# Performance work log

Hardware: AMD Instinct MI355X
Metric: run time of the kernel (lower is better)

Reference implementation:

```python
import jax, jax.numpy as jnp
import numpy as np

NUM_EXPERTS = 16
IN_FEATURES = 512
OUT_FEATURES = 512
N_TOKENS = 2048


def setup_inputs() -> dict:
    key = jax.random.key(0)
    k_x, k_idx, k_w, k_b = jax.random.split(key, 4)
    x = jax.random.normal(k_x, (N_TOKENS, IN_FEATURES), dtype=jnp.float32)
    indices = jax.random.randint(k_idx, (N_TOKENS,), 0, NUM_EXPERTS, dtype=jnp.int64)
    # nn.Linear default init: U(-1/sqrt(in), 1/sqrt(in)) for weight [out,in] and bias [out]
    bound = 1.0 / np.sqrt(IN_FEATURES)
    W = jax.random.uniform(k_w, (NUM_EXPERTS, OUT_FEATURES, IN_FEATURES),
                           minval=-bound, maxval=bound, dtype=jnp.float32)
    b = jax.random.uniform(k_b, (NUM_EXPERTS, OUT_FEATURES),
                           minval=-bound, maxval=bound, dtype=jnp.float32)
    return {"x": x, "indices": indices, "W": W, "b": b}


def reference(x, indices, W, b):
    # Faithful to SwitchLinear.forward: gather per-token expert weight/bias,
    # then per-token GEMV (batched matmul with a length-1 row dim).
    w_tok = W[indices]            # [N, out, in]  (naive per-token weight gather)
    b_tok = b[indices]            # [N, out]
    out = jnp.einsum('ni,noi->no', x, w_tok) + b_tok  # [N, out]
    return out
```

## Files before the change

### kernel.cpp

```cpp
#include <hip/hip_runtime.h>
#include <hip/hip_bf16.h>

#define NE    16
#define INF   512
#define OUTF  512
#define NT    2048
#define OTILE 32
#define TCH   64
#define WROWS OTILE
#define LSTRIDE 520

#define SZ_W   (WROWS * LSTRIDE * 2)
#define SZ_X   (TCH * LSTRIDE * 2)
#define SZ_LST ((NT + TCH) * 4)
#define SMEM_BYTES (SZ_W + SZ_X + SZ_LST + 32)

typedef __attribute__((ext_vector_type(4))) float f32x4;
typedef __attribute__((ext_vector_type(8))) short bf16x8;
typedef __attribute__((ext_vector_type(4))) short bf16x4;

__device__ inline short f2bf(float f) {
    union { __hip_bfloat16 h; short s; } u;
    u.h = __float2bfloat16(f);
    return u.s;
}

__device__ inline bf16x4 cvt4(f32x4 v) {
    bf16x4 r;
    r[0] = f2bf(v[0]); r[1] = f2bf(v[1]); r[2] = f2bf(v[2]); r[3] = f2bf(v[3]);
    return r;
}

__global__ __launch_bounds__(512, 2)
void switch_linear_kernel(const float* __restrict__ x,
                          const int* __restrict__ idx,
                          const float* __restrict__ W,
                          const float* __restrict__ bias,
                          float* __restrict__ out)
{
    extern __shared__ char smem[];
    short* s_W    = (short*)smem;
    short* s_X    = (short*)(smem + SZ_W);
    int*   s_list = (int*)(smem + SZ_W + SZ_X);
    int*   s_wcnt = (int*)(smem + SZ_W + SZ_X + SZ_LST);

    const int b   = blockIdx.x;
    const int e   = b & 15;
    const int oj  = (b >> 4) & 15;
    const int o0  = oj * OTILE;
    const int tid = threadIdx.x;
    const int lane = tid & 63;
    const int wid  = tid >> 6;

    int iv[4];
#pragma unroll
    for (int it = 0; it < 4; ++it)
        iv[it] = idx[wid * 256 + it * 64 + lane];

    const float* wbase = W + ((size_t)e * OUTF + o0) * INF;
#pragma unroll
    for (int i = 0; i < 8; ++i) {
        const int li = tid + i * 512;
        f32x4 v = ((const f32x4*)wbase)[li];
        const int fidx = li * 4;
        const int row = fidx >> 9;
        const int col = fidx & 511;
        *(bf16x4*)(&s_W[row * LSTRIDE + col]) = cvt4(v);
    }

    unsigned long long masks[4];
    int wtot = 0;
#pragma unroll
    for (int it = 0; it < 4; ++it) {
        const unsigned long long mk = __ballot(iv[it] == e);
        masks[it] = mk;
        wtot += __popcll(mk);
    }
    if (lane == 0) s_wcnt[wid] = wtot;
    __syncthreads();
    int base = 0;
#pragma unroll
    for (int w = 0; w < 8; ++w) { int c = s_wcnt[w]; if (w < wid) base += c; }
    const int cnt = s_wcnt[0] + s_wcnt[1] + s_wcnt[2] + s_wcnt[3]
                  + s_wcnt[4] + s_wcnt[5] + s_wcnt[6] + s_wcnt[7];
    const unsigned long long below = (1ull << lane) - 1ull;
    int run = base;
#pragma unroll
    for (int it = 0; it < 4; ++it) {
        const unsigned long long mk = masks[it];
        if (mk & (1ull << lane))
            s_list[run + __popcll(mk & below)] = wid * 256 + it * 64 + lane;
        run += __popcll(mk);
    }
    const int cnt_pad = (cnt + TCH - 1) & ~(TCH - 1);
    for (int i = cnt + tid; i < cnt_pad; i += 512) s_list[i] = -1;
    __syncthreads();
    if (cnt == 0) return;

    const int wt = wid >> 1;
    const int wo = wid & 1;
    const int lr = lane & 15;
    const int q  = lane >> 4;
    const int orow = o0 + wo * 16 + lr;

    bf16x8 bfr[16];
#pragma unroll
    for (int kk = 0; kk < 16; ++kk)
        bfr[kk] = *(const bf16x8*)(&s_W[(wo * 16 + lr) * LSTRIDE + kk * 32 + q * 8]);
    const float bv = bias[e * OUTF + orow];

    const int slot = tid >> 3;
    const int sub  = tid & 7;

    const int M = cnt_pad / TCH;
    int m0 = oj % M;
    for (int k = 0; k < M; ++k) {
        int m = m0 + k; if (m >= M) m -= M;
        const int cb = m * TCH;

        int tok_s = s_list[cb + slot];
        if (tok_s < 0) tok_s = 0;
        const f32x4* xr = (const f32x4*)(x + (size_t)tok_s * INF);
#pragma unroll
        for (int i = 0; i < 16; ++i) {
            f32x4 v = xr[sub + i * 8];
            *(bf16x4*)(&s_X[slot * LSTRIDE + sub * 4 + i * 32]) = cvt4(v);
        }
        __syncthreads();

        f32x4 acc = {0.f, 0.f, 0.f, 0.f};
#pragma unroll
        for (int kk = 0; kk < 16; ++kk) {
            bf16x8 afr = *(const bf16x8*)(&s_X[(wt * 16 + lr) * LSTRIDE + kk * 32 + q * 8]);
            acc = __builtin_amdgcn_mfma_f32_16x16x32_bf16(afr, bfr[kk], acc, 0, 0, 0);
        }
#pragma unroll
        for (int j = 0; j < 4; ++j) {
            const int tok = s_list[cb + wt * 16 + q * 4 + j];
            if (tok >= 0) out[(size_t)tok * OUTF + orow] = acc[j] + bv;
        }
        __syncthreads();
    }
}

extern "C" void kernel_launch(void* const* d_in, const int* in_sizes, int n_in,
                              void* d_out, int out_size, void* d_ws, size_t ws_size,
                              hipStream_t stream) {
    const float* x    = (const float*)d_in[0];
    const int*   idx  = (const int*)d_in[1];
    const float* W    = (const float*)d_in[2];
    const float* bias = (const float*)d_in[3];
    float* out = (float*)d_out;

    dim3 grid(NE * (OUTF / OTILE));
    dim3 block(512);
    switch_linear_kernel<<<grid, block, SMEM_BYTES, stream>>>(x, idx, W, bias, out);
}
```

Before: 14.24 us.

## Split token chunks across two blocks per expert tile with smaller blocks

Doubles the grid by adding a z dimension that splits each expert's token chunks between two blocks, halving block size to 256 threads and chunk size to 32 tokens. Each block still converts the full 32x512 weight tile and scans all indices, so that work is duplicated. The x loads are batched into registers before conversion to expose more memory parallelism, and the final barrier is skipped. The aim is more concurrent blocks and shorter per-block serial chains, at the cost of redundant weight staging and index scanning.

```diff
diff --git a/kernel.cpp b/kernel.cpp
--- a/kernel.cpp
+++ b/kernel.cpp
@@ -6,32 +6,33 @@
 #define OUTF  512
 #define NT    2048
 #define OTILE 32
-#define TCH   64
-#define WROWS OTILE
+#define TCH   32
+#define NZ    2
 #define LSTRIDE 520
 
-#define SZ_W   (WROWS * LSTRIDE * 2)
+#define SZ_W   (OTILE * LSTRIDE * 2)
 #define SZ_X   (TCH * LSTRIDE * 2)
 #define SZ_LST ((NT + TCH) * 4)
-#define SMEM_BYTES (SZ_W + SZ_X + SZ_LST + 32)
+#define SMEM_BYTES (SZ_W + SZ_X + SZ_LST + 64)
 
 typedef __attribute__((ext_vector_type(4))) float f32x4;
 typedef __attribute__((ext_vector_type(8))) short bf16x8;
 typedef __attribute__((ext_vector_type(4))) short bf16x4;
 
-__device__ inline short f2bf(float f) {
-    union { __hip_bfloat16 h; short s; } u;
+__device__ inline unsigned short f2bf(float f) {
+    union { __hip_bfloat16 h; unsigned short s; } u;
     u.h = __float2bfloat16(f);
     return u.s;
 }
 
 __device__ inline bf16x4 cvt4(f32x4 v) {
     bf16x4 r;
-    r[0] = f2bf(v[0]); r[1] = f2bf(v[1]); r[2] = f2bf(v[2]); r[3] = f2bf(v[3]);
+    r[0] = (short)f2bf(v[0]); r[1] = (short)f2bf(v[1]);
+    r[2] = (short)f2bf(v[2]); r[3] = (short)f2bf(v[3]);
     return r;
 }
 
-__global__ __launch_bounds__(512, 2)
+__global__ __launch_bounds__(256, 2)
 void switch_linear_kernel(const float* __restrict__ x,
                           const int* __restrict__ idx,
                           const float* __restrict__ W,
@@ -48,57 +49,56 @@
     const int e   = b & 15;
     const int oj  = (b >> 4) & 15;
     const int o0  = oj * OTILE;
+    const int z   = b >> 8;
     const int tid = threadIdx.x;
     const int lane = tid & 63;
-    const int wid  = tid >> 6;
+    const int wv   = tid >> 6;
 
-    int iv[4];
+    int iv[8];
 #pragma unroll
-    for (int it = 0; it < 4; ++it)
-        iv[it] = idx[wid * 256 + it * 64 + lane];
+    for (int it = 0; it < 8; ++it)
+        iv[it] = idx[wv * 512 + it * 64 + lane];
 
     const float* wbase = W + ((size_t)e * OUTF + o0) * INF;
 #pragma unroll
-    for (int i = 0; i < 8; ++i) {
-        const int li = tid + i * 512;
+    for (int i = 0; i < 16; ++i) {
+        const int li = tid + i * 256;
         f32x4 v = ((const f32x4*)wbase)[li];
-        const int fidx = li * 4;
-        const int row = fidx >> 9;
-        const int col = fidx & 511;
+        const int row = li >> 7;
+        const int col = (li * 4) & 511;
         *(bf16x4*)(&s_W[row * LSTRIDE + col]) = cvt4(v);
     }
 
-    unsigned long long masks[4];
+    unsigned long long masks[8];
     int wtot = 0;
 #pragma unroll
-    for (int it = 0; it < 4; ++it) {
+    for (int it = 0; it < 8; ++it) {
         const unsigned long long mk = __ballot(iv[it] == e);
         masks[it] = mk;
         wtot += __popcll(mk);
     }
-    if (lane == 0) s_wcnt[wid] = wtot;
+    if (lane == 0) s_wcnt[wv] = wtot;
     __syncthreads();
     int base = 0;
 #pragma unroll
-    for (int w = 0; w < 8; ++w) { int c = s_wcnt[w]; if (w < wid) base += c; }
-    const int cnt = s_wcnt[0] + s_wcnt[1] + s_wcnt[2] + s_wcnt[3]
-                  + s_wcnt[4] + s_wcnt[5] + s_wcnt[6] + s_wcnt[7];
+    for (int w = 0; w < 4; ++w) { int c = s_wcnt[w]; if (w < wv) base += c; }
+    const int cnt = s_wcnt[0] + s_wcnt[1] + s_wcnt[2] + s_wcnt[3];
     const unsigned long long below = (1ull << lane) - 1ull;
     int run = base;
 #pragma unroll
-    for (int it = 0; it < 4; ++it) {
+    for (int it = 0; it < 8; ++it) {
         const unsigned long long mk = masks[it];
         if (mk & (1ull << lane))
-            s_list[run + __popcll(mk & below)] = wid * 256 + it * 64 + lane;
+            s_list[run + __popcll(mk & below)] = wv * 512 + it * 64 + lane;
         run += __popcll(mk);
     }
     const int cnt_pad = (cnt + TCH - 1) & ~(TCH - 1);
-    for (int i = cnt + tid; i < cnt_pad; i += 512) s_list[i] = -1;
+    for (int i = cnt + tid; i < cnt_pad; i += 256) s_list[i] = -1;
     __syncthreads();
     if (cnt == 0) return;
 
-    const int wt = wid >> 1;
-    const int wo = wid & 1;
+    const int wt = wv >> 1;
+    const int wo = wv & 1;
     const int lr = lane & 15;
     const int q  = lane >> 4;
     const int orow = o0 + wo * 16 + lr;
@@ -112,20 +112,24 @@
     const int slot = tid >> 3;
     const int sub  = tid & 7;
 
-    const int M = cnt_pad / TCH;
-    int m0 = oj % M;
+    const int nch = cnt_pad / TCH;
+    const int M = (nch - z + NZ - 1) / NZ;
+    if (M <= 0) return;
+    const int m0 = oj % M;
+
     for (int k = 0; k < M; ++k) {
         int m = m0 + k; if (m >= M) m -= M;
-        const int cb = m * TCH;
+        const int cb = (z + m * NZ) * TCH;
 
         int tok_s = s_list[cb + slot];
         if (tok_s < 0) tok_s = 0;
         const f32x4* xr = (const f32x4*)(x + (size_t)tok_s * INF);
+        f32x4 xreg[16];
 #pragma unroll
-        for (int i = 0; i < 16; ++i) {
-            f32x4 v = xr[sub + i * 8];
-            *(bf16x4*)(&s_X[slot * LSTRIDE + sub * 4 + i * 32]) = cvt4(v);
-        }
+        for (int i = 0; i < 16; ++i) xreg[i] = xr[sub + i * 8];
+#pragma unroll
+        for (int i = 0; i < 16; ++i)
+            *(bf16x4*)(&s_X[slot * LSTRIDE + (sub + i * 8) * 4]) = cvt4(xreg[i]);
         __syncthreads();
 
         f32x4 acc = {0.f, 0.f, 0.f, 0.f};
@@ -139,7 +143,7 @@
             const int tok = s_list[cb + wt * 16 + q * 4 + j];
             if (tok >= 0) out[(size_t)tok * OUTF + orow] = acc[j] + bv;
         }
-        __syncthreads();
+        if (k != M - 1) __syncthreads();
     }
 }
 
@@ -152,7 +156,7 @@
     const float* bias = (const float*)d_in[3];
     float* out = (float*)d_out;
 
-    dim3 grid(NE * (OUTF / OTILE));
-    dim3 block(512);
+    dim3 grid(NE * 16 * NZ);
+    dim3 block(256);
     switch_linear_kernel<<<grid, block, SMEM_BYTES, stream>>>(x, idx, W, bias, out);
 }
```

After: 12.97 us, median of 2. 1.1x faster.
